# Performance work log

Measured on AMD Instinct MI355X. Metric: run time of the kernel, lower is better.

Reference implementation:

```python
import jax, jax.numpy as jnp
import numpy as np
from jax import lax

VOCAB = 32000
D_MODEL = 768
N_LAYERS = 2
D_STATE = 16
EXPAND = 2
D_CONV = 4
DT_RANK = 48
D_INNER = EXPAND * D_MODEL
B, L = 2, 1024
EPS = 1e-5


def rmsnorm(x, w):
    return x * lax.rsqrt(jnp.mean(x * x, axis=-1, keepdims=True) + EPS) * w


def selective_scan(deltaA, deltaBx, C):
    # deltaA, deltaBx: (B, L, ED, N); C: (B, L, N)
    h0 = jnp.zeros((deltaA.shape[0], deltaA.shape[2], deltaA.shape[3]), deltaA.dtype)

    def step(h, inp):
        dA, dBx, c = inp
        h = dA * h + dBx                      # (B, ED, N)
        y = jnp.einsum('ben,bn->be', h, c)    # (B, ED)
        return h, y

    xs = (deltaA.transpose(1, 0, 2, 3), deltaBx.transpose(1, 0, 2, 3), C.transpose(1, 0, 2))
    _, ys = lax.scan(step, h0, xs)            # (L, B, ED)
    return ys.transpose(1, 0, 2)


def mamba_block(x, in_w, conv_w, conv_b, xproj_w, dt_w, dt_b, A_log, Dp, out_w):
    # x: (B, L, D)
    xz = jnp.einsum('bld,ed->ble', x, in_w)               # (B, L, 2*ED)
    xa, z = jnp.split(xz, 2, axis=-1)
    # depthwise causal conv over time
    xc = xa.transpose(0, 2, 1)                            # (B, ED, L)
    kern = conv_w[:, None, :]                             # (ED, 1, d_conv)
    xc = lax.conv_general_dilated(xc, kern, (1,), [(D_CONV - 1, 0)],
                                  dimension_numbers=('NCH', 'OIH', 'NCH'),
                                  feature_group_count=D_INNER)
    xa = jax.nn.silu((xc + conv_b[None, :, None]).transpose(0, 2, 1))  # (B, L, ED)
    # ssm params
    dbc = jnp.einsum('ble,re->blr', xa, xproj_w)          # (B, L, dt_rank+2N)
    delta, Bm, Cm = jnp.split(dbc, [DT_RANK, DT_RANK + D_STATE], axis=-1)
    delta = jax.nn.softplus(jnp.einsum('blr,er->ble', delta, dt_w) + dt_b)  # (B, L, ED)
    A = -jnp.exp(A_log)                                   # (ED, N)
    deltaA = jnp.exp(delta[..., None] * A)                # (B, L, ED, N)
    deltaBx = delta[..., None] * Bm[:, :, None, :] * xa[..., None]
    y = selective_scan(deltaA, deltaBx, Cm) + Dp * xa     # (B, L, ED)
    y = y * jax.nn.silu(z)
    return jnp.einsum('ble,de->bld', y, out_w)            # (B, L, D)


def setup_inputs() -> dict:
    key = jax.random.key(0)
    ks = jax.random.split(key, 16)
    s = 0.02
    inp = {}
    inp['x'] = jax.random.randint(ks[0], (B, L), 0, VOCAB)
    inp['embed_W'] = jax.random.normal(ks[1], (VOCAB, D_MODEL), jnp.float32) * s
    inp['norm_w'] = jnp.ones((N_LAYERS, D_MODEL), jnp.float32)
    inp['in_proj_w'] = jax.random.normal(ks[2], (N_LAYERS, 2 * D_INNER, D_MODEL), jnp.float32) * s
    inp['conv_w'] = jax.random.normal(ks[3], (N_LAYERS, D_INNER, D_CONV), jnp.float32) * 0.2
    inp['conv_b'] = jnp.zeros((N_LAYERS, D_INNER), jnp.float32)
    inp['x_proj_w'] = jax.random.normal(ks[4], (N_LAYERS, DT_RANK + 2 * D_STATE, D_INNER), jnp.float32) * s
    inp['dt_proj_w'] = jax.random.normal(ks[5], (N_LAYERS, D_INNER, DT_RANK), jnp.float32) * (DT_RANK ** -0.5)
    inp['dt_proj_b'] = jnp.log(jnp.expm1(jnp.full((N_LAYERS, D_INNER), 0.01, jnp.float32)))
    inp['A_log'] = jnp.log(jnp.broadcast_to(jnp.arange(1, D_STATE + 1, dtype=jnp.float32), (N_LAYERS, D_INNER, D_STATE)))
    inp['D_param'] = jnp.ones((N_LAYERS, D_INNER), jnp.float32)
    inp['out_proj_w'] = jax.random.normal(ks[6], (N_LAYERS, D_MODEL, D_INNER), jnp.float32) * s
    inp['normf_w'] = jnp.ones((D_MODEL,), jnp.float32)
    inp['head_w'] = jax.random.normal(ks[7], (VOCAB, D_MODEL), jnp.float32) * s
    inp['head_b'] = jnp.zeros((VOCAB,), jnp.float32)
    return inp


def reference(x, embed_W, norm_w, in_proj_w, conv_w, conv_b, x_proj_w,
              dt_proj_w, dt_proj_b, A_log, D_param, out_proj_w,
              normf_w, head_w, head_b):
    h = embed_W[x]                                        # (B, L, D)
    for i in range(N_LAYERS):
        h = h + mamba_block(rmsnorm(h, norm_w[i]), in_proj_w[i], conv_w[i],
                            conv_b[i], x_proj_w[i], dt_proj_w[i], dt_proj_b[i],
                            A_log[i], D_param[i], out_proj_w[i])
    h = rmsnorm(h, normf_w)
    logits = jnp.einsum('bld,vd->blv', h, head_w) + head_b
    return logits
```

## Files before the change

kernel.cpp:

```cpp
#include <hip/hip_runtime.h>
#include <cmath>

constexpr int DM     = 768;
constexpr int DI     = 1536;
constexpr int DI2    = 3072;
constexpr int DSTATE = 16;
constexpr int DTRANK = 48;
constexpr int NDBC   = 80;
constexpr int BB     = 2;
constexpr int LL     = 1024;
constexpr int NT     = BB * LL;
constexpr int NVOCAB = 32000;
constexpr float EPSF = 1e-5f;
constexpr float LOG2E = 1.4426950408889634f;

constexpr int NC = 64;
constexpr int CL = LL / NC;

typedef unsigned short ushort_t;
typedef __bf16 bf16x8 __attribute__((ext_vector_type(8)));
typedef float  f32x4  __attribute__((ext_vector_type(4)));

__device__ inline ushort_t f2bf(float x) {
    unsigned int u = __builtin_bit_cast(unsigned int, x);
    unsigned int r = (u + 0x7FFFu + ((u >> 16) & 1u)) >> 16;
    return (ushort_t)r;
}

__global__ __launch_bounds__(256) void f2b_kernel(const float* __restrict__ in,
                                                  ushort_t* __restrict__ out, int n4) {
    int i = blockIdx.x * blockDim.x + threadIdx.x;
    if (i >= n4) return;
    float4 v = ((const float4*)in)[i];
    ushort4 o;
    o.x = f2bf(v.x); o.y = f2bf(v.y); o.z = f2bf(v.z); o.w = f2bf(v.w);
    ((ushort4*)out)[i] = o;
}

__global__ void embed_kernel(const int* __restrict__ x, const float* __restrict__ W,
                             float* __restrict__ h) {
    int t = blockIdx.x;
    int row = x[t];
    const float4* src = (const float4*)(W + (size_t)row * DM);
    float4* dst = (float4*)(h + (size_t)t * DM);
    for (int i = threadIdx.x; i < DM / 4; i += blockDim.x) dst[i] = src[i];
}

__global__ __launch_bounds__(256) void rmsnorm_kernel(const float* __restrict__ x,
                                                      const float* __restrict__ w,
                                                      ushort_t* __restrict__ o) {
    int t = blockIdx.x;
    const float* xr = x + (size_t)t * DM;
    float s = 0.f;
    for (int i = threadIdx.x; i < DM; i += 256) { float v = xr[i]; s += v * v; }
    #pragma unroll
    for (int off = 32; off >= 1; off >>= 1) s += __shfl_down(s, off, 64);
    __shared__ float wsum[4];
    if ((threadIdx.x & 63) == 0) wsum[threadIdx.x >> 6] = s;
    __syncthreads();
    float tot = wsum[0] + wsum[1] + wsum[2] + wsum[3];
    float r = rsqrtf(tot / DM + EPSF);
    ushort_t* orow = o + (size_t)t * DM;
    for (int i = threadIdx.x; i < DM; i += 256) orow[i] = f2bf(xr[i] * r * w[i]);
}

__device__ inline void gl_lds16(const void* g, void* l) {
    auto gp = (const __attribute__((address_space(1))) void*)(unsigned long long)(uintptr_t)g;
    auto lp = (__attribute__((address_space(3))) void*)(unsigned int)(uintptr_t)l;
    __builtin_amdgcn_global_load_lds(gp, lp, 16, 0, 0);
}

__global__ __launch_bounds__(256) void bgemm_bt(const ushort_t* __restrict__ A, int lda,
                                                const ushort_t* __restrict__ W, int ldw,
                                                float* __restrict__ C, int ldc,
                                                int K,
                                                const float* __restrict__ bias,
                                                const float* __restrict__ resid) {
    __shared__ ushort_t As[2][128 * 32];
    __shared__ ushort_t Bs[2][128 * 32];

    const int GX  = gridDim.x;
    const int nwg = GX * gridDim.y;
    int orig = blockIdx.y * GX + blockIdx.x;
    int q = nwg >> 3, r = nwg & 7, xcd = orig & 7, lq = orig >> 3;
    int wg = (xcd < r ? xcd * (q + 1) : r * (q + 1) + (xcd - r) * q) + lq;
    const int m0 = (wg % GX) * 128;
    const int n0 = (wg / GX) * 128;

    const int wave = threadIdx.x >> 6;
    const int lane = threadIdx.x & 63;
    const int lrow = lane >> 2;

    f32x4 acc[4][4] = {};

    const ushort_t* Ab = A + (size_t)m0 * lda;
    const ushort_t* Wb = W + (size_t)n0 * ldw;
    const int wm = (wave >> 1) * 64;
    const int wn = (wave & 1) * 64;

    auto stage = [&](int buf, int k0) {
        #pragma unroll
        for (int rr = 0; rr < 2; ++rr) {
            const int rowbase = rr * 64 + wave * 16;
            const int row = rowbase + lrow;
            const int csw = (((lane & 3) ^ ((row >> 1) & 3)) << 3);
            gl_lds16(Ab + (size_t)row * lda + k0 + csw, (char*)As[buf] + rowbase * 64);
            gl_lds16(Wb + (size_t)row * ldw + k0 + csw, (char*)Bs[buf] + rowbase * 64);
        }
    };

    const int S = K >> 5;
    stage(0, 0);
    stage(1, 32);

    const int rsw = ((lane >> 1) & 3);
    for (int s = 0; s < S; ++s) {
        if (s < S - 1) asm volatile("s_waitcnt vmcnt(4)" ::: "memory");
        else           asm volatile("s_waitcnt vmcnt(0)" ::: "memory");
        __builtin_amdgcn_s_barrier();

        const int cur = s & 1;
        bf16x8 af[4], bfr[4];
        const int rchunk = (((lane >> 4) ^ rsw) << 4);
        #pragma unroll
        for (int i = 0; i < 4; ++i) {
            af[i]  = *(const bf16x8*)((char*)As[cur] + (wm + i * 16 + (lane & 15)) * 64 + rchunk);
            bfr[i] = *(const bf16x8*)((char*)Bs[cur] + (wn + i * 16 + (lane & 15)) * 64 + rchunk);
        }
        asm volatile("s_waitcnt lgkmcnt(0)" ::: "memory");
        __builtin_amdgcn_sched_barrier(0);
        __builtin_amdgcn_s_barrier();
        if (s + 2 < S) stage(cur, (s + 2) << 5);

        __builtin_amdgcn_s_setprio(1);
        #pragma unroll
        for (int i = 0; i < 4; ++i)
            #pragma unroll
            for (int j = 0; j < 4; ++j)
                acc[i][j] = __builtin_amdgcn_mfma_f32_16x16x32_bf16(af[i], bfr[j], acc[i][j], 0, 0, 0);
        __builtin_amdgcn_s_setprio(0);
    }

    const int cn = lane & 15;
    const int cr = (lane >> 4) * 4;
    #pragma unroll
    for (int i = 0; i < 4; ++i) {
        #pragma unroll
        for (int j = 0; j < 4; ++j) {
            const int col = n0 + wn + j * 16 + cn;
            const float bv = bias ? bias[col] : 0.f;
            #pragma unroll
            for (int rr = 0; rr < 4; ++rr) {
                const int row = m0 + wm + i * 16 + cr + rr;
                const size_t idx = (size_t)row * ldc + col;
                float v = acc[i][j][rr] + bv;
                if (resid) v += resid[idx];
                C[idx] = v;
            }
        }
    }
}

constexpr int BM = 64, BN = 64, BK = 16;
__global__ __launch_bounds__(256) void sgemm_bt(const float* __restrict__ A, int lda,
                                                const float* __restrict__ W, int ldw,
                                                float* __restrict__ C, int ldc,
                                                int M, int N, int K,
                                                const float* __restrict__ bias,
                                                const float* __restrict__ resid,
                                                int act) {
    __shared__ float As[BK][BM];
    __shared__ float Ws[BK][BN];
    const int m0 = blockIdx.x * BM;
    const int n0 = blockIdx.y * BN;
    const int nz = gridDim.z;
    const int Kc = K / nz;
    const int kbeg = blockIdx.z * Kc;
    const int kend = kbeg + Kc;
    const int tid = threadIdx.x;
    const int tn = tid & 15, tm = tid >> 4;
    const int lr = tid >> 2;
    const int lk = (tid & 3) * 4;

    float acc[4][4] = {};

    for (int k0 = kbeg; k0 < kend; k0 += BK) {
        {
            float4 v = *(const float4*)(A + (size_t)(m0 + lr) * lda + k0 + lk);
            As[lk + 0][lr] = v.x; As[lk + 1][lr] = v.y;
            As[lk + 2][lr] = v.z; As[lk + 3][lr] = v.w;
            int n = n0 + lr;
            float4 u = make_float4(0.f, 0.f, 0.f, 0.f);
            if (n < N) u = *(const float4*)(W + (size_t)n * ldw + k0 + lk);
            Ws[lk + 0][lr] = u.x; Ws[lk + 1][lr] = u.y;
            Ws[lk + 2][lr] = u.z; Ws[lk + 3][lr] = u.w;
        }
        __syncthreads();
        #pragma unroll
        for (int kk = 0; kk < BK; ++kk) {
            float4 a = *(const float4*)&As[kk][tm * 4];
            float4 w = *(const float4*)&Ws[kk][tn * 4];
            acc[0][0] += a.x * w.x; acc[0][1] += a.x * w.y; acc[0][2] += a.x * w.z; acc[0][3] += a.x * w.w;
            acc[1][0] += a.y * w.x; acc[1][1] += a.y * w.y; acc[1][2] += a.y * w.z; acc[1][3] += a.y * w.w;
            acc[2][0] += a.z * w.x; acc[2][1] += a.z * w.y; acc[2][2] += a.z * w.z; acc[2][3] += a.z * w.w;
            acc[3][0] += a.w * w.x; acc[3][1] += a.w * w.y; acc[3][2] += a.w * w.z; acc[3][3] += a.w * w.w;
        }
        __syncthreads();
    }

    #pragma unroll
    for (int i = 0; i < 4; ++i) {
        int m = m0 + tm * 4 + i;
        #pragma unroll
        for (int j = 0; j < 4; ++j) {
            int n = n0 + tn * 4 + j;
            if (n < N) {
                const size_t idx = (size_t)m * ldc + n;
                float v = acc[i][j];
                if (nz > 1) {
                    atomicAdd(&C[idx], v);
                } else {
                    if (bias)  v += bias[n];
                    if (resid) v += resid[idx];
                    if (act == 1) v = (v > 20.f) ? v : log1pf(expf(v));
                    C[idx] = v;
                }
            }
        }
    }
}

__global__ void conv_silu_kernel(const float* __restrict__ xz, const float* __restrict__ cw,
                                 const float* __restrict__ cb, float* __restrict__ xa,
                                 float* __restrict__ dbc0) {
    int idx = blockIdx.x * blockDim.x + threadIdx.x;
    if (idx < NT * NDBC) dbc0[idx] = 0.f;
    if (idx >= NT * DI) return;
    int e = idx % DI;
    int t = idx / DI;
    int l = t & (LL - 1);
    float acc = cb[e];
    #pragma unroll
    for (int k = 0; k < 4; ++k) {
        int ll = l - 3 + k;
        if (ll >= 0) acc += cw[e * 4 + k] * xz[(size_t)(t - 3 + k) * DI2 + e];
    }
    xa[idx] = acc / (1.f + expf(-acc));
}


__global__ __launch_bounds__(256) void scan_carry(const float* __restrict__ delta,
                                                  const float* __restrict__ xa,
                                                  const float* __restrict__ dbc,
                                                  const float* __restrict__ A_log,
                                                  float* __restrict__ Ds,
                                                  float* __restrict__ Hc) {
    const int e = blockIdx.x * 256 + threadIdx.x;
    const int c = blockIdx.y;
    const int b = blockIdx.z;
    float aen[DSTATE], h[DSTATE];
    #pragma unroll
    for (int n = 0; n < DSTATE; ++n) {
        aen[n] = -expf(A_log[e * DSTATE + n]) * LOG2E;
        h[n] = 0.f;
    }
    float dsum = 0.f;
    const int t0 = b * LL + c * CL;
    const float* dp = delta + (size_t)t0 * DI + e;
    const float* xp = xa    + (size_t)t0 * DI + e;
    const float* bp = dbc   + (size_t)t0 * NDBC + DTRANK;
    for (int l = 0; l < CL; ++l) {
        float d  = dp[(size_t)l * DI];
        float xv = xp[(size_t)l * DI];
        const float* br = bp + (size_t)l * NDBC;
        dsum += d;
        float dxv = d * xv;
        #pragma unroll
        for (int n = 0; n < DSTATE; ++n) {
            float dA = exp2f(d * aen[n]);
            h[n] = dA * h[n] + dxv * br[n];
        }
    }
    const size_t cbase = ((size_t)(b * NC + c) * DI + e) * DSTATE;
    #pragma unroll
    for (int n = 0; n < DSTATE; ++n) Hc[cbase + n] = h[n];
    Ds[(size_t)(b * NC + c) * DI + e] = dsum;
}

__global__ __launch_bounds__(256) void scan_compose(const float* __restrict__ Ds,
                                                    const float* __restrict__ A_log,
                                                    float* __restrict__ Hc) {
    const int id = blockIdx.x * 256 + threadIdx.x;
    const int b = id / (DI * DSTATE);
    const int r = id - b * (DI * DSTATE);
    const int e = r >> 4;
    const float aen = -expf(A_log[r]) * LOG2E;
    float cur = 0.f;
    for (int c = 0; c < NC; ++c) {
        const size_t base = (size_t)(b * NC + c) * DI;
        float p  = exp2f(aen * Ds[base + e]);
        const size_t idx = base * DSTATE + r;
        float hl = Hc[idx];
        Hc[idx] = cur;
        cur = p * cur + hl;
    }
}

__global__ __launch_bounds__(256) void scan_apply(const float* __restrict__ delta,
                                                  const float* __restrict__ xa,
                                                  const float* __restrict__ dbc,
                                                  const float* __restrict__ xz,
                                                  const float* __restrict__ A_log,
                                                  const float* __restrict__ Dp,
                                                  const float* __restrict__ Hc,
                                                  ushort_t* __restrict__ ys) {
    const int e = blockIdx.x * 256 + threadIdx.x;
    const int c = blockIdx.y;
    const int b = blockIdx.z;
    float aen[DSTATE], h[DSTATE];
    const size_t cbase = ((size_t)(b * NC + c) * DI + e) * DSTATE;
    #pragma unroll
    for (int n = 0; n < DSTATE; ++n) {
        aen[n] = -expf(A_log[e * DSTATE + n]) * LOG2E;
        h[n] = Hc[cbase + n];
    }
    const float dpe = Dp[e];
    const int t0 = b * LL + c * CL;
    const float* dp = delta + (size_t)t0 * DI + e;
    const float* xp = xa    + (size_t)t0 * DI + e;
    const float* bp = dbc   + (size_t)t0 * NDBC + DTRANK;
    const float* zp = xz    + (size_t)t0 * DI2 + DI + e;
    ushort_t*    yp = ys    + (size_t)t0 * DI + e;
    for (int l = 0; l < CL; ++l) {
        float d  = dp[(size_t)l * DI];
        float xv = xp[(size_t)l * DI];
        const float* br = bp + (size_t)l * NDBC;
        const float* cr = br + DSTATE;
        float dxv = d * xv;
        float y = 0.f;
        #pragma unroll
        for (int n = 0; n < DSTATE; ++n) {
            float dA = exp2f(d * aen[n]);
            h[n] = dA * h[n] + dxv * br[n];
            y += h[n] * cr[n];
        }
        float z = zp[(size_t)l * DI2];
        float sz = z / (1.f + expf(-z));
        yp[(size_t)l * DI] = f2bf((y + dpe * xv) * sz);
    }
}

extern "C" void kernel_launch(void* const* d_in, const int* in_sizes, int n_in,
                              void* d_out, int out_size, void* d_ws, size_t ws_size,
                              hipStream_t stream) {
    const int*   x        = (const int*)  d_in[0];
    const float* embed_W  = (const float*)d_in[1];
    const float* norm_w   = (const float*)d_in[2];
    const float* in_w     = (const float*)d_in[3];
    const float* conv_w   = (const float*)d_in[4];
    const float* conv_b   = (const float*)d_in[5];
    const float* xproj_w  = (const float*)d_in[6];
    const float* dt_w     = (const float*)d_in[7];
    const float* dt_b     = (const float*)d_in[8];
    const float* A_log    = (const float*)d_in[9];
    const float* D_param  = (const float*)d_in[10];
    const float* out_w    = (const float*)d_in[11];
    const float* normf_w  = (const float*)d_in[12];
    const float* head_w   = (const float*)d_in[13];
    const float* head_b   = (const float*)d_in[14];
    float* logits = (float*)d_out;

    float* ws    = (float*)d_ws;
    float* h     = ws;
    float* xz    = h     + (size_t)NT * DM;
    float* xa    = xz    + (size_t)NT * DI2;
    float* dbc   = xa    + (size_t)NT * DI;
    float* delta = dbc   + (size_t)NT * NDBC;
    ushort_t* in_wb  = (ushort_t*)(delta + (size_t)NT * DI);
    ushort_t* out_wb = in_wb  + (size_t)2 * DI2 * DM;
    ushort_t* xnb    = out_wb + (size_t)2 * DM * DI;
    ushort_t* ys16   = xnb    + (size_t)NT * DM;
    float* Ds = (float*)(ys16 + (size_t)NT * DI);
    float* Hc = Ds + (size_t)BB * NC * DI;
    ushort_t* head_wb = (ushort_t*)xz;

    embed_kernel<<<NT, 192, 0, stream>>>(x, embed_W, h);

    {
        int n4 = 2 * DI2 * DM / 4;
        f2b_kernel<<<(n4 + 255) / 256, 256, 0, stream>>>(in_w, in_wb, n4);
        n4 = 2 * DM * DI / 4;
        f2b_kernel<<<(n4 + 255) / 256, 256, 0, stream>>>(out_w, out_wb, n4);
    }

    for (int i = 0; i < 2; ++i) {
        rmsnorm_kernel<<<NT, 256, 0, stream>>>(h, norm_w + (size_t)i * DM, xnb);
        bgemm_bt<<<dim3(NT / 128, DI2 / 128), 256, 0, stream>>>(
            xnb, DM, in_wb + (size_t)i * DI2 * DM, DM, xz, DI2, DM, nullptr, nullptr);
        conv_silu_kernel<<<(NT * DI + 255) / 256, 256, 0, stream>>>(
            xz, conv_w + (size_t)i * DI * 4, conv_b + (size_t)i * DI, xa, dbc);
        sgemm_bt<<<dim3(NT / BM, (NDBC + BN - 1) / BN, 8), 256, 0, stream>>>(
            xa, DI, xproj_w + (size_t)i * NDBC * DI, DI, dbc, NDBC,
            NT, NDBC, DI, nullptr, nullptr, 0);
        sgemm_bt<<<dim3(NT / BM, DI / BN), 256, 0, stream>>>(
            dbc, NDBC, dt_w + (size_t)i * DI * DTRANK, DTRANK, delta, DI,
            NT, DI, DTRANK, dt_b + (size_t)i * DI, nullptr, 1);
        scan_carry<<<dim3(DI / 256, NC, BB), 256, 0, stream>>>(
            delta, xa, dbc, A_log + (size_t)i * DI * DSTATE, Ds, Hc);
        scan_compose<<<(BB * DI * DSTATE) / 256, 256, 0, stream>>>(
            Ds, A_log + (size_t)i * DI * DSTATE, Hc);
        scan_apply<<<dim3(DI / 256, NC, BB), 256, 0, stream>>>(
            delta, xa, dbc, xz, A_log + (size_t)i * DI * DSTATE,
            D_param + (size_t)i * DI, Hc, ys16);
        bgemm_bt<<<dim3(NT / 128, DM / 128), 256, 0, stream>>>(
            ys16, DI, out_wb + (size_t)i * DM * DI, DI, h, DM, DI, nullptr, h);
    }

    rmsnorm_kernel<<<NT, 256, 0, stream>>>(h, normf_w, xnb);
    {
        int n4 = NVOCAB * DM / 4;
        f2b_kernel<<<(n4 + 255) / 256, 256, 0, stream>>>(head_w, head_wb, n4);
    }
    bgemm_bt<<<dim3(NT / 128, NVOCAB / 128), 256, 0, stream>>>(
        xnb, DM, head_wb, DM, logits, NVOCAB, DM, head_b, nullptr);
}
```

Before: 921.1 us.

## Add split-K with atomic accumulation to in_proj and out_proj bf16 GEMMs

The bf16 GEMM gains split-K over gridDim.z, with partial tiles accumulated into the output via float atomicAdd. The in_proj GEMM uses 2 K-splits, and its output buffer is zeroed inside the rmsnorm kernel. The out_proj GEMM uses 4 K-splits and accumulates directly into the residual stream h, which replaces the separate residual read. The aim is more workgroups for these small grids (16x24 and 16x6 tiles) on a large-CU GPU, at the cost of atomic traffic, extra zero-fill writes and a non-deterministic summation order.

```diff
diff --git a/kernel.cpp b/kernel.cpp
--- a/kernel.cpp
+++ b/kernel.cpp
@@ -48,8 +48,14 @@
 
 __global__ __launch_bounds__(256) void rmsnorm_kernel(const float* __restrict__ x,
                                                       const float* __restrict__ w,
-                                                      ushort_t* __restrict__ o) {
+                                                      ushort_t* __restrict__ o,
+                                                      float* __restrict__ zfill) {
     int t = blockIdx.x;
+    if (zfill) {
+        float4* zr = (float4*)(zfill + (size_t)t * DI2);
+        #pragma unroll
+        for (int i = 0; i < 3; ++i) zr[threadIdx.x + i * 256] = make_float4(0.f, 0.f, 0.f, 0.f);
+    }
     const float* xr = x + (size_t)t * DM;
     float s = 0.f;
     for (int i = threadIdx.x; i < DM; i += 256) { float v = xr[i]; s += v * v; }
@@ -87,14 +93,18 @@
     const int m0 = (wg % GX) * 128;
     const int n0 = (wg / GX) * 128;
 
+    const int nz   = gridDim.z;
+    const int Kc   = K / nz;
+    const int kbeg = blockIdx.z * Kc;
+
     const int wave = threadIdx.x >> 6;
     const int lane = threadIdx.x & 63;
     const int lrow = lane >> 2;
 
     f32x4 acc[4][4] = {};
 
-    const ushort_t* Ab = A + (size_t)m0 * lda;
-    const ushort_t* Wb = W + (size_t)n0 * ldw;
+    const ushort_t* Ab = A + (size_t)m0 * lda + kbeg;
+    const ushort_t* Wb = W + (size_t)n0 * ldw + kbeg;
     const int wm = (wave >> 1) * 64;
     const int wn = (wave & 1) * 64;
 
@@ -109,7 +119,7 @@
         }
     };
 
-    const int S = K >> 5;
+    const int S = Kc >> 5;
     stage(0, 0);
     stage(1, 32);
 
@@ -148,14 +158,18 @@
         #pragma unroll
         for (int j = 0; j < 4; ++j) {
             const int col = n0 + wn + j * 16 + cn;
-            const float bv = bias ? bias[col] : 0.f;
+            const float bv = (nz == 1 && bias) ? bias[col] : 0.f;
             #pragma unroll
             for (int rr = 0; rr < 4; ++rr) {
                 const int row = m0 + wm + i * 16 + cr + rr;
                 const size_t idx = (size_t)row * ldc + col;
-                float v = acc[i][j][rr] + bv;
-                if (resid) v += resid[idx];
-                C[idx] = v;
+                if (nz > 1) {
+                    atomicAdd(&C[idx], acc[i][j][rr]);
+                } else {
+                    float v = acc[i][j][rr] + bv;
+                    if (resid) v += resid[idx];
+                    C[idx] = v;
+                }
             }
         }
     }
@@ -394,8 +408,8 @@
     }
 
     for (int i = 0; i < 2; ++i) {
-        rmsnorm_kernel<<<NT, 256, 0, stream>>>(h, norm_w + (size_t)i * DM, xnb);
-        bgemm_bt<<<dim3(NT / 128, DI2 / 128), 256, 0, stream>>>(
+        rmsnorm_kernel<<<NT, 256, 0, stream>>>(h, norm_w + (size_t)i * DM, xnb, xz);
+        bgemm_bt<<<dim3(NT / 128, DI2 / 128, 2), 256, 0, stream>>>(
             xnb, DM, in_wb + (size_t)i * DI2 * DM, DM, xz, DI2, DM, nullptr, nullptr);
         conv_silu_kernel<<<(NT * DI + 255) / 256, 256, 0, stream>>>(
             xz, conv_w + (size_t)i * DI * 4, conv_b + (size_t)i * DI, xa, dbc);
@@ -412,11 +426,11 @@
         scan_apply<<<dim3(DI / 256, NC, BB), 256, 0, stream>>>(
             delta, xa, dbc, xz, A_log + (size_t)i * DI * DSTATE,
             D_param + (size_t)i * DI, Hc, ys16);
-        bgemm_bt<<<dim3(NT / 128, DM / 128), 256, 0, stream>>>(
-            ys16, DI, out_wb + (size_t)i * DM * DI, DI, h, DM, DI, nullptr, h);
-    }
-
-    rmsnorm_kernel<<<NT, 256, 0, stream>>>(h, normf_w, xnb);
+        bgemm_bt<<<dim3(NT / 128, DM / 128, 4), 256, 0, stream>>>(
+            ys16, DI, out_wb + (size_t)i * DM * DI, DI, h, DM, DI, nullptr, nullptr);
+    }
+
+    rmsnorm_kernel<<<NT, 256, 0, stream>>>(h, normf_w, xnb, nullptr);
     {
         int n4 = NVOCAB * DM / 4;
         f2b_kernel<<<(n4 + 255) / 256, 256, 0, stream>>>(head_w, head_wb, n4);
```

Measured after the change: 1.008 ms. +9.4%, slower.
